# Kernel tuning notes

Measured on AMD Instinct MI355X. Metric: run time of the kernel, lower is better.

## Reference

```python
import jax, jax.numpy as jnp
import numpy as np

H = 6  # hidden size == input size

def setup_inputs() -> dict:
    key = jax.random.key(0)
    ks = jax.random.split(key, 14)
    B, T = 8192, 512
    s_in = 1.0 / np.sqrt(H)
    inp = {
        "x": jax.random.normal(ks[0], (B, T, H), dtype=jnp.float32),
        # PyTorch LSTM param layout: w_ih [4H, in], w_hh [4H, H], gate order i,f,g,o
        "w_ih_0": jax.random.uniform(ks[1], (4 * H, H), jnp.float32, -s_in, s_in),
        "w_hh_0": jax.random.uniform(ks[2], (4 * H, H), jnp.float32, -s_in, s_in),
        "b_ih_0": jax.random.uniform(ks[3], (4 * H,), jnp.float32, -s_in, s_in),
        "b_hh_0": jax.random.uniform(ks[4], (4 * H,), jnp.float32, -s_in, s_in),
        "w_ih_1": jax.random.uniform(ks[5], (4 * H, H), jnp.float32, -s_in, s_in),
        "w_hh_1": jax.random.uniform(ks[6], (4 * H, H), jnp.float32, -s_in, s_in),
        "b_ih_1": jax.random.uniform(ks[7], (4 * H,), jnp.float32, -s_in, s_in),
        "b_hh_1": jax.random.uniform(ks[8], (4 * H,), jnp.float32, -s_in, s_in),
        "fc1_w": jax.random.uniform(ks[9], (32, H), jnp.float32, -s_in, s_in),
        "fc1_b": jax.random.uniform(ks[10], (32,), jnp.float32, -s_in, s_in),
        "fc2_w": jax.random.uniform(ks[11], (1, 32), jnp.float32, -1 / np.sqrt(32), 1 / np.sqrt(32)),
        "fc2_b": jax.random.uniform(ks[12], (1,), jnp.float32, -1 / np.sqrt(32), 1 / np.sqrt(32)),
    }
    return inp


def _lstm_cell(x_t, h, c, w_ih, w_hh, b):
    # gates: [B, 4H]; PyTorch order i, f, g, o
    gates = x_t @ w_ih.T + h @ w_hh.T + b
    i, f, g, o = jnp.split(gates, 4, axis=-1)
    i = jax.nn.sigmoid(i)
    f = jax.nn.sigmoid(f)
    g = jnp.tanh(g)
    o = jax.nn.sigmoid(o)
    c_new = f * c + i * g
    h_new = o * jnp.tanh(c_new)
    return h_new, c_new


def reference(x, w_ih_0, w_hh_0, b_ih_0, b_hh_0, w_ih_1, w_hh_1, b_ih_1, b_hh_1,
              fc1_w, fc1_b, fc2_w, fc2_b):
    B, T, _ = x.shape
    b0 = b_ih_0 + b_hh_0
    b1 = b_ih_1 + b_hh_1
    zeros = jnp.zeros((B, H), dtype=x.dtype)

    def step(carry, x_t):
        h0, c0, h1, c1 = carry
        h0, c0 = _lstm_cell(x_t, h0, c0, w_ih_0, w_hh_0, b0)
        h1, c1 = _lstm_cell(h0, h1, c1, w_ih_1, w_hh_1, b1)
        return (h0, c0, h1, c1), h1

    xs = jnp.swapaxes(x, 0, 1)  # [T, B, H]
    _, ys = jax.lax.scan(step, (zeros, zeros, zeros, zeros), xs)
    out = jnp.swapaxes(ys, 0, 1)  # [B, T, H]

    # eval-mode: dropout is identity
    out = jax.nn.relu(out @ fc1_w.T + fc1_b)
    out = jax.nn.relu(out @ fc2_w.T + fc2_b)
    return out  # [B, T, 1]
```

## Files before the change

kernel.cpp:

```cpp
#include <hip/hip_runtime.h>


typedef float v2f __attribute__((ext_vector_type(2)));

static constexpr float L2E  = 1.44269504088896340736f;
static constexpr float TL2E = 2.0f * L2E;

#define DPP_X1 0xB1
#define DPP_X2 0x4E
#define DPP_X8 0x128

template<int CTRL>
__device__ __forceinline__ float dppf(float v) {
    return __int_as_float(__builtin_amdgcn_update_dpp(
        0, __float_as_int(v), CTRL, 0xF, 0xF, true));
}

#define PIN(v) asm volatile("" : "+v"(v))

__device__ __forceinline__ float sig_pre(float a) {
    return __builtin_amdgcn_rcpf(1.0f + __builtin_amdgcn_exp2f(a));
}
__device__ __forceinline__ float tanh_pre(float a) {
    return fmaf(-2.0f, __builtin_amdgcn_rcpf(1.0f + __builtin_amdgcn_exp2f(a)), 1.0f);
}

extern "C" __global__ void __launch_bounds__(64)
__attribute__((amdgpu_waves_per_eu(1, 1)))
lstm_dpp8(const float* __restrict__ x,
          const float* __restrict__ wih0, const float* __restrict__ whh0,
          const float* __restrict__ bih0, const float* __restrict__ bhh0,
          const float* __restrict__ wih1, const float* __restrict__ whh1,
          const float* __restrict__ bih1, const float* __restrict__ bhh1,
          const float* __restrict__ fc1w, const float* __restrict__ fc1b,
          const float* __restrict__ fc2w, const float* __restrict__ fc2b,
          float* __restrict__ out, int nbatch)
{
    const int L   = threadIdx.x;
    const int l   = L & 15;
    const int row = L >> 4;
    const int cst = (l >> 2) & 1;
    const int p   = (l & 3) | ((l >> 3) << 2);

    int seq = blockIdx.x * 8 + row * 2 + cst;
    const bool live = (seq < nbatch);
    if (!live) seq = nbatch - 1;

    const float km = (p < 6) ? 1.0f : 0.0f;
    const int   k  = (p < 6) ? p : 0;
    const int ir = k, fr = 6 + k, gr = 12 + k, orr = 18 + k;

    v2f wiA0[6], wiB0[6];
#pragma unroll
    for (int j = 0; j < 6; ++j) {
        wiA0[j] = (v2f){ wih0[ir*6+j]*(-L2E)*km,  wih0[fr*6+j]*(-L2E)*km };
        wiB0[j] = (v2f){ wih0[gr*6+j]*( TL2E)*km, wih0[orr*6+j]*(-L2E)*km };
    }
    v2f whA0[8], whB0[8], wiA1[8], wiB1[8], whA1[8], whB1[8], f1wA[8], f1wB[8];
#pragma unroll
    for (int s = 0; s < 8; ++s) {
        const int   u  = p ^ s;
        const float cm = (u < 6) ? km   : 0.0f;
        const float fm = (u < 6) ? 1.0f : 0.0f;
        const int   uc = (u < 6) ? u    : 0;
        whA0[s] = (v2f){ whh0[ir*6+uc]*(-L2E)*cm,  whh0[fr*6+uc]*(-L2E)*cm };
        whB0[s] = (v2f){ whh0[gr*6+uc]*( TL2E)*cm, whh0[orr*6+uc]*(-L2E)*cm };
        wiA1[s] = (v2f){ wih1[ir*6+uc]*(-L2E)*cm,  wih1[fr*6+uc]*(-L2E)*cm };
        wiB1[s] = (v2f){ wih1[gr*6+uc]*( TL2E)*cm, wih1[orr*6+uc]*(-L2E)*cm };
        whA1[s] = (v2f){ whh1[ir*6+uc]*(-L2E)*cm,  whh1[fr*6+uc]*(-L2E)*cm };
        whB1[s] = (v2f){ whh1[gr*6+uc]*( TL2E)*cm, whh1[orr*6+uc]*(-L2E)*cm };
        f1wA[s] = (v2f){ fc1w[(4*p+0)*6+uc]*fm, fc1w[(4*p+1)*6+uc]*fm };
        f1wB[s] = (v2f){ fc1w[(4*p+2)*6+uc]*fm, fc1w[(4*p+3)*6+uc]*fm };
    }
    v2f bbA0 = (v2f){ (bih0[ir]+bhh0[ir])*(-L2E)*km,  (bih0[fr]+bhh0[fr])*(-L2E)*km };
    v2f bbB0 = (v2f){ (bih0[gr]+bhh0[gr])*( TL2E)*km, (bih0[orr]+bhh0[orr])*(-L2E)*km };
    v2f bbA1 = (v2f){ (bih1[ir]+bhh1[ir])*(-L2E)*km,  (bih1[fr]+bhh1[fr])*(-L2E)*km };
    v2f bbB1 = (v2f){ (bih1[gr]+bhh1[gr])*( TL2E)*km, (bih1[orr]+bhh1[orr])*(-L2E)*km };
    v2f f1bA = (v2f){ fc1b[4*p+0], fc1b[4*p+1] };
    v2f f1bB = (v2f){ fc1b[4*p+2], fc1b[4*p+3] };
    v2f f2wA = (v2f){ fc2w[4*p+0], fc2w[4*p+1] };
    v2f f2wB = (v2f){ fc2w[4*p+2], fc2w[4*p+3] };
    float f2b = fc2b[0];

#pragma unroll
    for (int j = 0; j < 6; ++j) { PIN(wiA0[j]); PIN(wiB0[j]); }
#pragma unroll
    for (int s = 0; s < 8; ++s) {
        PIN(whA0[s]); PIN(whB0[s]); PIN(wiA1[s]); PIN(wiB1[s]);
        PIN(whA1[s]); PIN(whB1[s]); PIN(f1wA[s]); PIN(f1wB[s]);
    }
    PIN(bbA0); PIN(bbB0); PIN(bbA1); PIN(bbB1);
    PIN(f1bA); PIN(f1bB); PIN(f2wA); PIN(f2wB); PIN(f2b);

    float h0s[8], h1s[8];
#pragma unroll
    for (int s = 0; s < 8; ++s) { h0s[s] = 0.0f; h1s[s] = 0.0f; }
    float c0 = 0.0f, c1 = 0.0f;

    const float* xp = x + (size_t)seq * (512 * 6);
    float*       op = out + (size_t)seq * 512;

    float2 xq[4][3];
#pragma unroll
    for (int j = 0; j < 4; ++j) {
        const float* q = xp + j * 6;
        xq[j][0] = *(const float2*)(q + 0);
        xq[j][1] = *(const float2*)(q + 2);
        xq[j][2] = *(const float2*)(q + 4);
    }

    const v2f Z2 = (v2f){0.0f, 0.0f};
    float y[4];

    for (int T = 0; T < 512; T += 4) {
        const int Tn = (T < 508) ? T + 4 : 508;
#pragma unroll
        for (int j = 0; j < 4; ++j) {
            const float* xr = xp + (Tn + j) * 6;
            float2 nx0 = *(const float2*)(xr + 0);
            float2 nx1 = *(const float2*)(xr + 2);
            float2 nx2 = *(const float2*)(xr + 4);

            v2f pA = bbA1, pAb = Z2, pB = bbB1, pBb = Z2;
#pragma unroll
            for (int s = 0; s < 8; s += 2) {
                pA  += whA1[s]   * h1s[s];
                pAb += whA1[s+1] * h1s[s+1];
                pB  += whB1[s]   * h1s[s];
                pBb += whB1[s+1] * h1s[s+1];
            }

            v2f aA = bbA0, aAb = Z2, aB = bbB0, aBb = Z2;
            aA  += wiA0[0] * xq[j][0].x;  aAb += wiA0[1] * xq[j][0].y;
            aA  += wiA0[2] * xq[j][1].x;  aAb += wiA0[3] * xq[j][1].y;
            aA  += wiA0[4] * xq[j][2].x;  aAb += wiA0[5] * xq[j][2].y;
            aB  += wiB0[0] * xq[j][0].x;  aBb += wiB0[1] * xq[j][0].y;
            aB  += wiB0[2] * xq[j][1].x;  aBb += wiB0[3] * xq[j][1].y;
            aB  += wiB0[4] * xq[j][2].x;  aBb += wiB0[5] * xq[j][2].y;
#pragma unroll
            for (int s = 0; s < 8; s += 2) {
                aA  += whA0[s]   * h0s[s];
                aAb += whA0[s+1] * h0s[s+1];
                aB  += whB0[s]   * h0s[s];
                aBb += whB0[s+1] * h0s[s+1];
            }
            v2f gA0 = aA + aAb, gB0 = aB + aBb;
            float i0 = sig_pre(gA0.x), f0 = sig_pre(gA0.y);
            float g0 = tanh_pre(gB0.x), o0 = sig_pre(gB0.y);
            c0 = fmaf(f0, c0, i0 * g0);
            float h0 = o0 * tanh_pre(TL2E * c0);

            h0s[0] = h0;
            h0s[1] = dppf<DPP_X1>(h0s[0]);
            h0s[2] = dppf<DPP_X2>(h0s[0]);
            h0s[3] = dppf<DPP_X2>(h0s[1]);
            h0s[4] = dppf<DPP_X8>(h0s[0]);
            h0s[5] = dppf<DPP_X8>(h0s[1]);
            h0s[6] = dppf<DPP_X8>(h0s[2]);
            h0s[7] = dppf<DPP_X8>(h0s[3]);

#pragma unroll
            for (int s = 0; s < 8; s += 2) {
                pA  += wiA1[s]   * h0s[s];
                pAb += wiA1[s+1] * h0s[s+1];
                pB  += wiB1[s]   * h0s[s];
                pBb += wiB1[s+1] * h0s[s+1];
            }
            v2f gA1 = pA + pAb, gB1 = pB + pBb;
            float i1 = sig_pre(gA1.x), f1 = sig_pre(gA1.y);
            float g1 = tanh_pre(gB1.x), o1 = sig_pre(gB1.y);
            c1 = fmaf(f1, c1, i1 * g1);
            float h1 = o1 * tanh_pre(TL2E * c1);

            h1s[0] = h1;
            h1s[1] = dppf<DPP_X1>(h1s[0]);
            h1s[2] = dppf<DPP_X2>(h1s[0]);
            h1s[3] = dppf<DPP_X2>(h1s[1]);
            h1s[4] = dppf<DPP_X8>(h1s[0]);
            h1s[5] = dppf<DPP_X8>(h1s[1]);
            h1s[6] = dppf<DPP_X8>(h1s[2]);
            h1s[7] = dppf<DPP_X8>(h1s[3]);

            v2f rA = f1bA, rAb = Z2, rB = f1bB, rBb = Z2;
#pragma unroll
            for (int s = 0; s < 8; s += 2) {
                rA  += f1wA[s]   * h1s[s];
                rAb += f1wA[s+1] * h1s[s+1];
                rB  += f1wB[s]   * h1s[s];
                rBb += f1wB[s+1] * h1s[s+1];
            }
            v2f RA = rA + rAb, RB = rB + rBb;
            RA.x = fmaxf(RA.x, 0.0f); RA.y = fmaxf(RA.y, 0.0f);
            RB.x = fmaxf(RB.x, 0.0f); RB.y = fmaxf(RB.y, 0.0f);
            float acc = RA.x * f2wA.x;
            acc = fmaf(RA.y, f2wA.y, acc);
            acc = fmaf(RB.x, f2wB.x, acc);
            acc = fmaf(RB.y, f2wB.y, acc);
            acc += dppf<DPP_X1>(acc);
            acc += dppf<DPP_X2>(acc);
            acc += dppf<DPP_X8>(acc);
            y[j] = fmaxf(acc + f2b, 0.0f);

            xq[j][0] = nx0; xq[j][1] = nx1; xq[j][2] = nx2;
        }
        if (live && ((L & 11) == 0)) {
            float4 yv = make_float4(y[0], y[1], y[2], y[3]);
            *(float4*)(op + T) = yv;
        }
    }
}

extern "C" void kernel_launch(void* const* d_in, const int* in_sizes, int n_in,
                              void* d_out, int out_size, void* d_ws, size_t ws_size,
                              hipStream_t stream) {
    const float* x     = (const float*)d_in[0];
    const float* wih0  = (const float*)d_in[1];
    const float* whh0  = (const float*)d_in[2];
    const float* bih0  = (const float*)d_in[3];
    const float* bhh0  = (const float*)d_in[4];
    const float* wih1  = (const float*)d_in[5];
    const float* whh1  = (const float*)d_in[6];
    const float* bih1  = (const float*)d_in[7];
    const float* bhh1  = (const float*)d_in[8];
    const float* fc1w  = (const float*)d_in[9];
    const float* fc1b  = (const float*)d_in[10];
    const float* fc2w  = (const float*)d_in[11];
    const float* fc2b  = (const float*)d_in[12];
    float* out = (float*)d_out;

    const int nbatch = in_sizes[0] / (512 * 6);
    const int grid   = (nbatch + 7) / 8;

    hipLaunchKernelGGL(lstm_dpp8, dim3(grid), dim3(64), 0, stream,
                       x, wih0, whh0, bih0, bhh0, wih1, whh1, bih1, bhh1,
                       fc1w, fc1b, fc2w, fc2b, out, nbatch);
}
```

Measured before the change: 202.2 us.

## Broadcast hidden state via DPP quad-broadcast and use packed FMA with op_sel

The old XOR-permuted 8-slot hidden-state exchange is replaced by a gather into three packed pairs, built with one row-shift DPP plus quad-broadcast DPPs. Weights are now stored in plain index order with 6 slots per gate instead of 8. Inline-asm v_pk_fma_f32 with op_sel picks the low or high half of each packed h pair, which cuts the FMA count per gate from 8 to 6 terms. The goal is fewer DPP moves and fewer FMAs on the serial recurrence, at the cost of extra lane selects and inline asm that the compiler cannot schedule around.

```diff
diff --git a/kernel.cpp b/kernel.cpp
--- a/kernel.cpp
+++ b/kernel.cpp
@@ -6,9 +6,14 @@
 static constexpr float L2E  = 1.44269504088896340736f;
 static constexpr float TL2E = 2.0f * L2E;
 
-#define DPP_X1 0xB1
-#define DPP_X2 0x4E
-#define DPP_X8 0x128
+#define DPP_QP(a,b,c,d) ((a)|((b)<<2)|((c)<<4)|((d)<<6))
+#define DPP_X1  DPP_QP(1,0,3,2)
+#define DPP_X2  DPP_QP(2,3,0,1)
+#define DPP_B0  DPP_QP(0,0,0,0)
+#define DPP_B1  DPP_QP(1,1,1,1)
+#define DPP_B2  DPP_QP(2,2,2,2)
+#define DPP_B3  DPP_QP(3,3,3,3)
+#define DPP_X8  0x128
 
 template<int CTRL>
 __device__ __forceinline__ float dppf(float v) {
@@ -18,6 +23,10 @@
 
 #define PIN(v) asm volatile("" : "+v"(v))
 
+#define PKFMA_LO(d,a,b) asm("v_pk_fma_f32 %0, %1, %2, %0 op_sel:[0,0,0] op_sel_hi:[1,0,1]" : "+v"(d) : "v"(a), "v"(b))
+#define PKFMA_HI(d,a,b) asm("v_pk_fma_f32 %0, %1, %2, %0 op_sel:[0,1,0] op_sel_hi:[1,1,1]" : "+v"(d) : "v"(a), "v"(b))
+#define PKADD(d,a,b)    asm("v_pk_add_f32 %0, %1, %2" : "=v"(d) : "v"(a), "v"(b))
+
 __device__ __forceinline__ float sig_pre(float a) {
     return __builtin_amdgcn_rcpf(1.0f + __builtin_amdgcn_exp2f(a));
 }
@@ -27,20 +36,21 @@
 
 extern "C" __global__ void __launch_bounds__(64)
 __attribute__((amdgpu_waves_per_eu(1, 1)))
-lstm_dpp8(const float* __restrict__ x,
-          const float* __restrict__ wih0, const float* __restrict__ whh0,
-          const float* __restrict__ bih0, const float* __restrict__ bhh0,
-          const float* __restrict__ wih1, const float* __restrict__ whh1,
-          const float* __restrict__ bih1, const float* __restrict__ bhh1,
-          const float* __restrict__ fc1w, const float* __restrict__ fc1b,
-          const float* __restrict__ fc2w, const float* __restrict__ fc2b,
-          float* __restrict__ out, int nbatch)
+lstm_dpp8v6(const float* __restrict__ x,
+            const float* __restrict__ wih0, const float* __restrict__ whh0,
+            const float* __restrict__ bih0, const float* __restrict__ bhh0,
+            const float* __restrict__ wih1, const float* __restrict__ whh1,
+            const float* __restrict__ bih1, const float* __restrict__ bhh1,
+            const float* __restrict__ fc1w, const float* __restrict__ fc1b,
+            const float* __restrict__ fc2w, const float* __restrict__ fc2b,
+            float* __restrict__ out, int nbatch)
 {
     const int L   = threadIdx.x;
     const int l   = L & 15;
     const int row = L >> 4;
     const int cst = (l >> 2) & 1;
     const int p   = (l & 3) | ((l >> 3) << 2);
+    const bool lowq = ((L >> 3) & 1) == 0;
 
     int seq = blockIdx.x * 8 + row * 2 + cst;
     const bool live = (seq < nbatch);
@@ -51,26 +61,19 @@
     const int ir = k, fr = 6 + k, gr = 12 + k, orr = 18 + k;
 
     v2f wiA0[6], wiB0[6];
+    v2f whA0[6], whB0[6], wiA1[6], wiB1[6], whA1[6], whB1[6], f1wA[6], f1wB[6];
 #pragma unroll
     for (int j = 0; j < 6; ++j) {
         wiA0[j] = (v2f){ wih0[ir*6+j]*(-L2E)*km,  wih0[fr*6+j]*(-L2E)*km };
         wiB0[j] = (v2f){ wih0[gr*6+j]*( TL2E)*km, wih0[orr*6+j]*(-L2E)*km };
-    }
-    v2f whA0[8], whB0[8], wiA1[8], wiB1[8], whA1[8], whB1[8], f1wA[8], f1wB[8];
-#pragma unroll
-    for (int s = 0; s < 8; ++s) {
-        const int   u  = p ^ s;
-        const float cm = (u < 6) ? km   : 0.0f;
-        const float fm = (u < 6) ? 1.0f : 0.0f;
-        const int   uc = (u < 6) ? u    : 0;
-        whA0[s] = (v2f){ whh0[ir*6+uc]*(-L2E)*cm,  whh0[fr*6+uc]*(-L2E)*cm };
-        whB0[s] = (v2f){ whh0[gr*6+uc]*( TL2E)*cm, whh0[orr*6+uc]*(-L2E)*cm };
-        wiA1[s] = (v2f){ wih1[ir*6+uc]*(-L2E)*cm,  wih1[fr*6+uc]*(-L2E)*cm };
-        wiB1[s] = (v2f){ wih1[gr*6+uc]*( TL2E)*cm, wih1[orr*6+uc]*(-L2E)*cm };
-        whA1[s] = (v2f){ whh1[ir*6+uc]*(-L2E)*cm,  whh1[fr*6+uc]*(-L2E)*cm };
-        whB1[s] = (v2f){ whh1[gr*6+uc]*( TL2E)*cm, whh1[orr*6+uc]*(-L2E)*cm };
-        f1wA[s] = (v2f){ fc1w[(4*p+0)*6+uc]*fm, fc1w[(4*p+1)*6+uc]*fm };
-        f1wB[s] = (v2f){ fc1w[(4*p+2)*6+uc]*fm, fc1w[(4*p+3)*6+uc]*fm };
+        whA0[j] = (v2f){ whh0[ir*6+j]*(-L2E)*km,  whh0[fr*6+j]*(-L2E)*km };
+        whB0[j] = (v2f){ whh0[gr*6+j]*( TL2E)*km, whh0[orr*6+j]*(-L2E)*km };
+        wiA1[j] = (v2f){ wih1[ir*6+j]*(-L2E)*km,  wih1[fr*6+j]*(-L2E)*km };
+        wiB1[j] = (v2f){ wih1[gr*6+j]*( TL2E)*km, wih1[orr*6+j]*(-L2E)*km };
+        whA1[j] = (v2f){ whh1[ir*6+j]*(-L2E)*km,  whh1[fr*6+j]*(-L2E)*km };
+        whB1[j] = (v2f){ whh1[gr*6+j]*( TL2E)*km, whh1[orr*6+j]*(-L2E)*km };
+        f1wA[j] = (v2f){ fc1w[(4*p+0)*6+j], fc1w[(4*p+1)*6+j] };
+        f1wB[j] = (v2f){ fc1w[(4*p+2)*6+j], fc1w[(4*p+3)*6+j] };
     }
     v2f bbA0 = (v2f){ (bih0[ir]+bhh0[ir])*(-L2E)*km,  (bih0[fr]+bhh0[fr])*(-L2E)*km };
     v2f bbB0 = (v2f){ (bih0[gr]+bhh0[gr])*( TL2E)*km, (bih0[orr]+bhh0[orr])*(-L2E)*km };
@@ -83,33 +86,42 @@
     float f2b = fc2b[0];
 
 #pragma unroll
-    for (int j = 0; j < 6; ++j) { PIN(wiA0[j]); PIN(wiB0[j]); }
-#pragma unroll
-    for (int s = 0; s < 8; ++s) {
-        PIN(whA0[s]); PIN(whB0[s]); PIN(wiA1[s]); PIN(wiB1[s]);
-        PIN(whA1[s]); PIN(whB1[s]); PIN(f1wA[s]); PIN(f1wB[s]);
+    for (int j = 0; j < 6; ++j) {
+        PIN(wiA0[j]); PIN(wiB0[j]); PIN(whA0[j]); PIN(whB0[j]);
+        PIN(wiA1[j]); PIN(wiB1[j]); PIN(whA1[j]); PIN(whB1[j]);
+        PIN(f1wA[j]); PIN(f1wB[j]);
     }
     PIN(bbA0); PIN(bbB0); PIN(bbA1); PIN(bbB1);
     PIN(f1bA); PIN(f1bB); PIN(f2wA); PIN(f2wB); PIN(f2b);
 
-    float h0s[8], h1s[8];
-#pragma unroll
-    for (int s = 0; s < 8; ++s) { h0s[s] = 0.0f; h1s[s] = 0.0f; }
+    v2f h0p[3], h1p[3];
+    const v2f Z2 = (v2f){0.0f, 0.0f};
+#pragma unroll
+    for (int q = 0; q < 3; ++q) { h0p[q] = Z2; h1p[q] = Z2; }
     float c0 = 0.0f, c1 = 0.0f;
 
     const float* xp = x + (size_t)seq * (512 * 6);
     float*       op = out + (size_t)seq * 512;
 
-    float2 xq[4][3];
+    v2f xq[4][3];
 #pragma unroll
     for (int j = 0; j < 4; ++j) {
         const float* q = xp + j * 6;
-        xq[j][0] = *(const float2*)(q + 0);
-        xq[j][1] = *(const float2*)(q + 2);
-        xq[j][2] = *(const float2*)(q + 4);
-    }
-
-    const v2f Z2 = (v2f){0.0f, 0.0f};
+        xq[j][0] = *(const v2f*)(q + 0);
+        xq[j][1] = *(const v2f*)(q + 2);
+        xq[j][2] = *(const v2f*)(q + 4);
+    }
+
+#define GATHER(HP_, HV_)                                                        \
+    {                                                                           \
+        float u_ = dppf<DPP_X8>(HV_);                     \
+        float hl = lowq ? (HV_) : u_;                 \
+        float hh = lowq ? u_ : (HV_);                 \
+        HP_[0] = (v2f){ dppf<DPP_B0>(hl), dppf<DPP_B1>(hl) };                   \
+        HP_[1] = (v2f){ dppf<DPP_B2>(hl), dppf<DPP_B3>(hl) };                   \
+        HP_[2] = (v2f){ dppf<DPP_B0>(hh), dppf<DPP_B1>(hh) };                   \
+    }
+
     float y[4];
 
     for (int T = 0; T < 512; T += 4) {
@@ -117,85 +129,73 @@
 #pragma unroll
         for (int j = 0; j < 4; ++j) {
             const float* xr = xp + (Tn + j) * 6;
-            float2 nx0 = *(const float2*)(xr + 0);
-            float2 nx1 = *(const float2*)(xr + 2);
-            float2 nx2 = *(const float2*)(xr + 4);
-
-            v2f pA = bbA1, pAb = Z2, pB = bbB1, pBb = Z2;
-#pragma unroll
-            for (int s = 0; s < 8; s += 2) {
-                pA  += whA1[s]   * h1s[s];
-                pAb += whA1[s+1] * h1s[s+1];
-                pB  += whB1[s]   * h1s[s];
-                pBb += whB1[s+1] * h1s[s+1];
-            }
-
-            v2f aA = bbA0, aAb = Z2, aB = bbB0, aBb = Z2;
-            aA  += wiA0[0] * xq[j][0].x;  aAb += wiA0[1] * xq[j][0].y;
-            aA  += wiA0[2] * xq[j][1].x;  aAb += wiA0[3] * xq[j][1].y;
-            aA  += wiA0[4] * xq[j][2].x;  aAb += wiA0[5] * xq[j][2].y;
-            aB  += wiB0[0] * xq[j][0].x;  aBb += wiB0[1] * xq[j][0].y;
-            aB  += wiB0[2] * xq[j][1].x;  aBb += wiB0[3] * xq[j][1].y;
-            aB  += wiB0[4] * xq[j][2].x;  aBb += wiB0[5] * xq[j][2].y;
-#pragma unroll
-            for (int s = 0; s < 8; s += 2) {
-                aA  += whA0[s]   * h0s[s];
-                aAb += whA0[s+1] * h0s[s+1];
-                aB  += whB0[s]   * h0s[s];
-                aBb += whB0[s+1] * h0s[s+1];
-            }
-            v2f gA0 = aA + aAb, gB0 = aB + aBb;
+            v2f nx0 = *(const v2f*)(xr + 0);
+            v2f nx1 = *(const v2f*)(xr + 2);
+            v2f nx2 = *(const v2f*)(xr + 4);
+
+            v2f pA = bbA1, pA2 = Z2, pB = bbB1, pB2 = Z2;
+            PKFMA_LO(pA, whA1[0], h1p[0]); PKFMA_HI(pA2, whA1[1], h1p[0]);
+            PKFMA_LO(pA, whA1[2], h1p[1]); PKFMA_HI(pA2, whA1[3], h1p[1]);
+            PKFMA_LO(pA, whA1[4], h1p[2]); PKFMA_HI(pA2, whA1[5], h1p[2]);
+            PKFMA_LO(pB, whB1[0], h1p[0]); PKFMA_HI(pB2, whB1[1], h1p[0]);
+            PKFMA_LO(pB, whB1[2], h1p[1]); PKFMA_HI(pB2, whB1[3], h1p[1]);
+            PKFMA_LO(pB, whB1[4], h1p[2]); PKFMA_HI(pB2, whB1[5], h1p[2]);
+
+            v2f aA = bbA0, aA2 = Z2, aB = bbB0, aB2 = Z2;
+            PKFMA_LO(aA, wiA0[0], xq[j][0]); PKFMA_HI(aA2, wiA0[1], xq[j][0]);
+            PKFMA_LO(aA, wiA0[2], xq[j][1]); PKFMA_HI(aA2, wiA0[3], xq[j][1]);
+            PKFMA_LO(aA, wiA0[4], xq[j][2]); PKFMA_HI(aA2, wiA0[5], xq[j][2]);
+            PKFMA_LO(aB, wiB0[0], xq[j][0]); PKFMA_HI(aB2, wiB0[1], xq[j][0]);
+            PKFMA_LO(aB, wiB0[2], xq[j][1]); PKFMA_HI(aB2, wiB0[3], xq[j][1]);
+            PKFMA_LO(aB, wiB0[4], xq[j][2]); PKFMA_HI(aB2, wiB0[5], xq[j][2]);
+            PKFMA_LO(aA, whA0[0], h0p[0]);  PKFMA_HI(aA2, whA0[1], h0p[0]);
+            PKFMA_LO(aA, whA0[2], h0p[1]);  PKFMA_HI(aA2, whA0[3], h0p[1]);
+            PKFMA_LO(aA, whA0[4], h0p[2]);  PKFMA_HI(aA2, whA0[5], h0p[2]);
+            PKFMA_LO(aB, whB0[0], h0p[0]);  PKFMA_HI(aB2, whB0[1], h0p[0]);
+            PKFMA_LO(aB, whB0[2], h0p[1]);  PKFMA_HI(aB2, whB0[3], h0p[1]);
+            PKFMA_LO(aB, whB0[4], h0p[2]);  PKFMA_HI(aB2, whB0[5], h0p[2]);
+            v2f gA0, gB0;
+            PKADD(gA0, aA, aA2);
+            PKADD(gB0, aB, aB2);
+
             float i0 = sig_pre(gA0.x), f0 = sig_pre(gA0.y);
             float g0 = tanh_pre(gB0.x), o0 = sig_pre(gB0.y);
             c0 = fmaf(f0, c0, i0 * g0);
             float h0 = o0 * tanh_pre(TL2E * c0);
 
-            h0s[0] = h0;
-            h0s[1] = dppf<DPP_X1>(h0s[0]);
-            h0s[2] = dppf<DPP_X2>(h0s[0]);
-            h0s[3] = dppf<DPP_X2>(h0s[1]);
-            h0s[4] = dppf<DPP_X8>(h0s[0]);
-            h0s[5] = dppf<DPP_X8>(h0s[1]);
-            h0s[6] = dppf<DPP_X8>(h0s[2]);
-            h0s[7] = dppf<DPP_X8>(h0s[3]);
-
-#pragma unroll
-            for (int s = 0; s < 8; s += 2) {
-                pA  += wiA1[s]   * h0s[s];
-                pAb += wiA1[s+1] * h0s[s+1];
-                pB  += wiB1[s]   * h0s[s];
-                pBb += wiB1[s+1] * h0s[s+1];
-            }
-            v2f gA1 = pA + pAb, gB1 = pB + pBb;
+            GATHER(h0p, h0);
+
+            PKFMA_LO(pA, wiA1[0], h0p[0]); PKFMA_HI(pA2, wiA1[1], h0p[0]);
+            PKFMA_LO(pA, wiA1[2], h0p[1]); PKFMA_HI(pA2, wiA1[3], h0p[1]);
+            PKFMA_LO(pA, wiA1[4], h0p[2]); PKFMA_HI(pA2, wiA1[5], h0p[2]);
+            PKFMA_LO(pB, wiB1[0], h0p[0]); PKFMA_HI(pB2, wiB1[1], h0p[0]);
+            PKFMA_LO(pB, wiB1[2], h0p[1]); PKFMA_HI(pB2, wiB1[3], h0p[1]);
+            PKFMA_LO(pB, wiB1[4], h0p[2]); PKFMA_HI(pB2, wiB1[5], h0p[2]);
+            v2f gA1, gB1;
+            PKADD(gA1, pA, pA2);
+            PKADD(gB1, pB, pB2);
+
             float i1 = sig_pre(gA1.x), f1 = sig_pre(gA1.y);
             float g1 = tanh_pre(gB1.x), o1 = sig_pre(gB1.y);
             c1 = fmaf(f1, c1, i1 * g1);
             float h1 = o1 * tanh_pre(TL2E * c1);
 
-            h1s[0] = h1;
-            h1s[1] = dppf<DPP_X1>(h1s[0]);
-            h1s[2] = dppf<DPP_X2>(h1s[0]);
-            h1s[3] = dppf<DPP_X2>(h1s[1]);
-            h1s[4] = dppf<DPP_X8>(h1s[0]);
-            h1s[5] = dppf<DPP_X8>(h1s[1]);
-            h1s[6] = dppf<DPP_X8>(h1s[2]);
-            h1s[7] = dppf<DPP_X8>(h1s[3]);
-
-            v2f rA = f1bA, rAb = Z2, rB = f1bB, rBb = Z2;
-#pragma unroll
-            for (int s = 0; s < 8; s += 2) {
-                rA  += f1wA[s]   * h1s[s];
-                rAb += f1wA[s+1] * h1s[s+1];
-                rB  += f1wB[s]   * h1s[s];
-                rBb += f1wB[s+1] * h1s[s+1];
-            }
-            v2f RA = rA + rAb, RB = rB + rBb;
-            RA.x = fmaxf(RA.x, 0.0f); RA.y = fmaxf(RA.y, 0.0f);
-            RB.x = fmaxf(RB.x, 0.0f); RB.y = fmaxf(RB.y, 0.0f);
-            float acc = RA.x * f2wA.x;
-            acc = fmaf(RA.y, f2wA.y, acc);
-            acc = fmaf(RB.x, f2wB.x, acc);
-            acc = fmaf(RB.y, f2wB.y, acc);
+            GATHER(h1p, h1);
+
+            v2f rA = f1bA, rA2 = Z2, rB = f1bB, rB2 = Z2;
+            PKFMA_LO(rA, f1wA[0], h1p[0]); PKFMA_HI(rA2, f1wA[1], h1p[0]);
+            PKFMA_LO(rA, f1wA[2], h1p[1]); PKFMA_HI(rA2, f1wA[3], h1p[1]);
+            PKFMA_LO(rA, f1wA[4], h1p[2]); PKFMA_HI(rA2, f1wA[5], h1p[2]);
+            PKFMA_LO(rB, f1wB[0], h1p[0]); PKFMA_HI(rB2, f1wB[1], h1p[0]);
+            PKFMA_LO(rB, f1wB[2], h1p[1]); PKFMA_HI(rB2, f1wB[3], h1p[1]);
+            PKFMA_LO(rB, f1wB[4], h1p[2]); PKFMA_HI(rB2, f1wB[5], h1p[2]);
+            v2f RA, RB;
+            PKADD(RA, rA, rA2);
+            PKADD(RB, rB, rB2);
+            float acc =          fmaxf(RA.x, 0.0f) * f2wA.x;
+            acc = fmaf(fmaxf(RA.y, 0.0f), f2wA.y, acc);
+            acc = fmaf(fmaxf(RB.x, 0.0f), f2wB.x, acc);
+            acc = fmaf(fmaxf(RB.y, 0.0f), f2wB.y, acc);
             acc += dppf<DPP_X1>(acc);
             acc += dppf<DPP_X2>(acc);
             acc += dppf<DPP_X8>(acc);
@@ -231,7 +231,7 @@
     const int nbatch = in_sizes[0] / (512 * 6);
     const int grid   = (nbatch + 7) / 8;
 
-    hipLaunchKernelGGL(lstm_dpp8, dim3(grid), dim3(64), 0, stream,
+    hipLaunchKernelGGL(lstm_dpp8v6, dim3(grid), dim3(64), 0, stream,
                        x, wih0, whh0, bih0, bhh0, wih1, whh1, bih1, bhh1,
                        fc1w, fc1b, fc2w, fc2b, out, nbatch);
 }
```

Result: no change. 199.0 us (-1.6%).
